# Kernel optimization log

Hardware: AMD Instinct MI355X
Metric: run time of the kernel (lower is better)

## Reference

```python
import jax, jax.numpy as jnp
import numpy as np

B, NQ, NKV, D, H, HD = 8, 1024, 2048, 1024, 16, 64  # inner_dim = H*HD = 1024


def setup_inputs() -> dict:
    key = jax.random.key(0)
    ks = jax.random.split(key, 10)
    s = 0.02
    return {
        "latent": jax.random.normal(ks[0], (B, NQ, D), jnp.float32),
        "data": jax.random.normal(ks[1], (B, NKV, D), jnp.float32),
        "wq": jax.random.normal(ks[2], (D, H * HD), jnp.float32) * s,
        "bq": jax.random.normal(ks[3], (H * HD,), jnp.float32) * s,
        "wk": jax.random.normal(ks[4], (D, H * HD), jnp.float32) * s,
        "bk": jax.random.normal(ks[5], (H * HD,), jnp.float32) * s,
        "wv": jax.random.normal(ks[6], (D, H * HD), jnp.float32) * s,
        "bv": jax.random.normal(ks[7], (H * HD,), jnp.float32) * s,
        "wo": jax.random.normal(ks[8], (H * HD, D), jnp.float32) * s,
        "bo": jax.random.normal(ks[9], (D,), jnp.float32) * s,
    }


def reference(latent, data, wq, bq, wk, bk, wv, bv, wo, bo):
    scale = HD ** -0.5
    # projections: [b, n, H*HD] -> [b, h, n, d]
    def split_heads(t):
        b, n, _ = t.shape
        return t.reshape(b, n, H, HD).transpose(0, 2, 1, 3)

    q = split_heads(latent @ wq + bq)   # [b, h, nq, d]
    k = split_heads(data @ wk + bk)     # [b, h, nkv, d]
    v = split_heads(data @ wv + bv)     # [b, h, nkv, d]

    scores = jnp.einsum("bhid,bhjd->bhij", q, k) * scale  # [b, h, nq, nkv]
    att = jax.nn.softmax(scores, axis=-1)                  # dropout p=0 (eval)
    out = jnp.einsum("bhij,bhjd->bhid", att, v)            # [b, h, nq, d]
    out = out.transpose(0, 2, 1, 3).reshape(B, NQ, H * HD)
    return out @ wo + bo
```

## Files before the change

### kernel.cpp

```cpp
#include <hip/hip_runtime.h>
#include <hip/hip_bf16.h>
#include <math.h>


using short8  = __attribute__((ext_vector_type(8))) short;
using f32x4   = __attribute__((ext_vector_type(4))) float;
using uint4v  = __attribute__((ext_vector_type(4))) unsigned int;

__device__ __forceinline__ ushort f2bf(float f) {
    unsigned u = __builtin_bit_cast(unsigned, f);
    u = (u + 0x7FFFu + ((u >> 16) & 1u)) >> 16;
    return (ushort)u;
}
__device__ __forceinline__ unsigned pack_bf2(float lo, float hi) {
    unsigned ulo = __builtin_bit_cast(unsigned, lo) + 0x8000u;
    unsigned uhi = __builtin_bit_cast(unsigned, hi) + 0x8000u;
    return __builtin_amdgcn_perm(uhi, ulo, 0x07060302);
}

__device__ __forceinline__ void gld_lds16(const ushort* g, ushort* l) {
    __builtin_amdgcn_global_load_lds(
        (const __attribute__((address_space(1))) unsigned int*)(const void*)g,
        (__attribute__((address_space(3))) unsigned int*)(void*)l,
        16, 0, 0);
}

__global__ void cvt_bf16(const float* __restrict__ in, ushort* __restrict__ out, int n) {
    int i = (blockIdx.x * blockDim.x + threadIdx.x) * 8;
    if (i >= n) return;
    float4 a = *(const float4*)(in + i);
    float4 b = *(const float4*)(in + i + 4);
    short8 o;
    o[0] = (short)f2bf(a.x); o[1] = (short)f2bf(a.y);
    o[2] = (short)f2bf(a.z); o[3] = (short)f2bf(a.w);
    o[4] = (short)f2bf(b.x); o[5] = (short)f2bf(b.y);
    o[6] = (short)f2bf(b.z); o[7] = (short)f2bf(b.w);
    *(short8*)(out + i) = o;
}

__global__ void transpose_w(const float* __restrict__ w0, const float* __restrict__ w1,
                            const float* __restrict__ w2, const float* __restrict__ w3,
                            ushort* __restrict__ o0, ushort* __restrict__ o1,
                            ushort* __restrict__ o2, ushort* __restrict__ o3) {
    __shared__ ushort tile[32][33];
    int z = blockIdx.z;
    const float* in = (z == 0) ? w0 : (z == 1) ? w1 : (z == 2) ? w2 : w3;
    ushort* out     = (z == 0) ? o0 : (z == 1) ? o1 : (z == 2) ? o2 : o3;
    int tx = threadIdx.x, ty = threadIdx.y;
    int x = blockIdx.x * 32 + tx;
    int y = blockIdx.y * 32;
#pragma unroll
    for (int i = 0; i < 32; i += 8)
        tile[ty + i][tx] = f2bf(in[(size_t)(y + ty + i) * 1024 + x]);
    __syncthreads();
    int x2 = blockIdx.y * 32 + tx;
    int y2 = blockIdx.x * 32;
#pragma unroll
    for (int i = 0; i < 32; i += 8)
        out[(size_t)(y2 + ty + i) * 1024 + x2] = tile[tx][ty + i];
}

template <int S>
__device__ __forceinline__ void stage_half(const ushort* __restrict__ G, int rbase,
                                           ushort* tile, int H, int kcol,
                                           int wave, int lane) {
#pragma unroll
    for (int c = 0; c < 2; ++c) {
        int rho = c * 64 + wave * 8;
        int gr0 = (rho / S) * (2 * S) + H * S + (rho % S);
        int rig = lane >> 3;
        int q   = (lane & 7) ^ rig;
        gld_lds16(G + (size_t)(rbase + gr0 + rig) * 1024 + kcol + q * 8,
                  tile + gr0 * 64);
    }
}

__device__ __forceinline__ void gemm256_body(
        const ushort* __restrict__ A, const ushort* __restrict__ Bt,
        const float* __restrict__ bias, void* __restrict__ Cv,
        float scale, int mode, int bm, int bn) {
    __shared__ __align__(16) ushort sm[65536];
    ushort* As0 = sm;
    ushort* Bs0 = sm + 16384;
    ushort* As1 = sm + 32768;
    ushort* Bs1 = sm + 49152;

    const int tid  = threadIdx.x;
    const int wave = tid >> 6, lane = tid & 63;
    const int l15 = lane & 15, quad = lane >> 4;
    const int wm = wave >> 2, wn = wave & 3;
    const int m0 = bm * 256, n0 = bn * 256;

    const int rA  = wm * 128 + l15;
    const int rB  = wn * 64 + l15;
    const int cq0 = quad ^ (l15 & 7);
    const int cq1 = (4 + quad) ^ (l15 & 7);

    stage_half<64>(A,  m0, As0, 0, 0,  wave, lane);
    stage_half<32>(Bt, n0, Bs0, 0, 0,  wave, lane);
    stage_half<32>(Bt, n0, Bs0, 1, 0,  wave, lane);
    stage_half<64>(A,  m0, As0, 1, 0,  wave, lane);
    stage_half<64>(A,  m0, As1, 0, 64, wave, lane);
    stage_half<32>(Bt, n0, Bs1, 1, 64, wave, lane);
    stage_half<64>(A,  m0, As1, 1, 64, wave, lane);
    asm volatile("s_waitcnt vmcnt(6)" ::: "memory");
    __builtin_amdgcn_s_barrier();

    f32x4 acc[8][4] = {};

#define LDA(MH)                                                                   \
    _Pragma("unroll")                                                             \
    for (int mi = 0; mi < 4; ++mi) {                                              \
        a[mi][0] = *(const short8*)(Ac + (rA + (MH) * 64 + mi * 16) * 64 + cq0 * 8); \
        a[mi][1] = *(const short8*)(Ac + (rA + (MH) * 64 + mi * 16) * 64 + cq1 * 8); \
    }
#define LDB(NH)                                                                   \
    _Pragma("unroll")                                                             \
    for (int ni = 0; ni < 2; ++ni) {                                              \
        b[ni][0] = *(const short8*)(Bc + (rB + (NH) * 32 + ni * 16) * 64 + cq0 * 8); \
        b[ni][1] = *(const short8*)(Bc + (rB + (NH) * 32 + ni * 16) * 64 + cq1 * 8); \
    }
#define MFMA_PHASE(MB, NB)                                                        \
    __builtin_amdgcn_s_barrier();                                                 \
    asm volatile("s_waitcnt lgkmcnt(0)" ::: "memory");                            \
    __builtin_amdgcn_sched_barrier(0);                                            \
    __builtin_amdgcn_s_setprio(1);                                                \
    _Pragma("unroll")                                                             \
    for (int mi = 0; mi < 4; ++mi)                                                \
        _Pragma("unroll")                                                         \
        for (int ni = 0; ni < 2; ++ni)                                            \
            _Pragma("unroll")                                                     \
            for (int kk = 0; kk < 2; ++kk)                                        \
                acc[(MB) * 4 + mi][(NB) * 2 + ni] =                               \
                    __builtin_amdgcn_mfma_f32_16x16x32_bf16(                      \
                        a[mi][kk], b[ni][kk], acc[(MB) * 4 + mi][(NB) * 2 + ni],  \
                        0, 0, 0);                                                 \
    __builtin_amdgcn_s_setprio(0);                                                \
    __builtin_amdgcn_s_barrier();

#pragma unroll 2
    for (int g = 0; g < 16; ++g) {
        ushort* Ac = (g & 1) ? As1 : As0;
        ushort* Bc = (g & 1) ? Bs1 : Bs0;
        ushort* Bn = (g & 1) ? Bs0 : Bs1;
        const int k1 = ((g + 1) & 15) * 64;
        const int k2 = ((g + 2) & 15) * 64;
        short8 a[4][2], b[2][2];

        LDA(0) LDB(0)
        stage_half<32>(Bt, n0, Bn, 0, k1, wave, lane);
        MFMA_PHASE(0, 0)

        LDB(1)
        stage_half<64>(A, m0, Ac, 0, k2, wave, lane);
        MFMA_PHASE(0, 1)

        LDA(1)
        stage_half<32>(Bt, n0, Bc, 1, k2, wave, lane);
        MFMA_PHASE(1, 1)

        LDB(0)
        stage_half<64>(A, m0, Ac, 1, k2, wave, lane);
        asm volatile("s_waitcnt vmcnt(6)" ::: "memory");
        MFMA_PHASE(1, 0)
    }
#undef LDA
#undef LDB
#undef MFMA_PHASE

    asm volatile("s_waitcnt vmcnt(0)" ::: "memory");

    float bvv[4];
    int   cols[4];
#pragma unroll
    for (int n4 = 0; n4 < 4; ++n4) {
        cols[n4] = n0 + wn * 64 + n4 * 16 + l15;
        bvv[n4]  = bias[cols[n4]];
    }
#pragma unroll
    for (int m8 = 0; m8 < 8; ++m8) {
        int rbase = m0 + wm * 128 + m8 * 16 + quad * 4;
#pragma unroll
        for (int n4 = 0; n4 < 4; ++n4) {
            float v[4];
#pragma unroll
            for (int rr = 0; rr < 4; ++rr)
                v[rr] = (acc[m8][n4][rr] + bvv[n4]) * scale;
            if (mode == 1) {
                int kvl = rbase & 2047;
                int pos = (kvl & ~31) + ((kvl >> 2) & 3) * 8 + ((kvl >> 4) & 1) * 4;
                size_t base = ((size_t)((rbase >> 11) * 1024 + cols[n4])) * 2048 + pos;
                uint2 o;
                o.x = pack_bf2(v[0], v[1]);
                o.y = pack_bf2(v[2], v[3]);
                *(uint2*)((ushort*)Cv + base) = o;
            } else if (mode == 0) {
#pragma unroll
                for (int rr = 0; rr < 4; ++rr)
                    ((ushort*)Cv)[(size_t)(rbase + rr) * 1024 + cols[n4]] = f2bf(v[rr]);
            } else {
#pragma unroll
                for (int rr = 0; rr < 4; ++rr)
                    ((float*)Cv)[(size_t)(rbase + rr) * 1024 + cols[n4]] = v[rr];
            }
        }
    }
}

__global__ __launch_bounds__(512, 2) void proj_qkv(
        const ushort* __restrict__ latB, const ushort* __restrict__ datB,
        const ushort* __restrict__ wqT, const ushort* __restrict__ wkT,
        const ushort* __restrict__ wvT,
        const float* __restrict__ bq, const float* __restrict__ bk,
        const float* __restrict__ bv,
        ushort* __restrict__ Qb, ushort* __restrict__ Kb, ushort* __restrict__ Vtb,
        float qscale) {
    int bid = ((int)blockIdx.x & 7) * 80 + ((int)blockIdx.x >> 3);
    const ushort* A;
    const ushort* W;
    const float*  bias;
    void*         C;
    float sc;
    int mode, idx;
    if (bid < 128)      { A = latB; W = wqT; bias = bq; C = Qb;  sc = qscale; mode = 0; idx = bid; }
    else if (bid < 384) { A = datB; W = wkT; bias = bk; C = Kb;  sc = 1.f;    mode = 0; idx = bid - 128; }
    else                { A = datB; W = wvT; bias = bv; C = Vtb; sc = 1.f;    mode = 1; idx = bid - 384; }
    gemm256_body(A, W, bias, C, sc, mode, idx >> 2, idx & 3);
}

template <int MODE>
__global__ void gemm_bt(const ushort* __restrict__ A, const ushort* __restrict__ Bt,
                        const float* __restrict__ bias, void* __restrict__ Cv,
                        int K, float scale) {
    __shared__ __align__(16) ushort As[128 * 32];
    __shared__ __align__(16) ushort Bs[128 * 32];
    const int tid  = threadIdx.x;
    const int wave = tid >> 6, lane = tid & 63;
    const int l15 = lane & 15, quad = lane >> 4;
    const int wm = wave & 1, wn = wave >> 1;
    const int m0 = blockIdx.x * 128;
    const int n0 = blockIdx.y * 128;

    f32x4 acc[4][4] = {};

    for (int k0 = 0; k0 < K; k0 += 32) {
        __syncthreads();
#pragma unroll
        for (int i = 0; i < 2; ++i) {
            int f   = (i * 256 + tid) * 8;
            int row = f >> 5, col = f & 31;
            gld_lds16(A  + (size_t)(m0 + row) * K + k0 + col, As + (i * 256 + wave * 64) * 8);
            gld_lds16(Bt + (size_t)(n0 + row) * K + k0 + col, Bs + (i * 256 + wave * 64) * 8);
        }
        __syncthreads();

        short8 a[4], b[4];
#pragma unroll
        for (int mi = 0; mi < 4; ++mi)
            a[mi] = *(const short8*)(As + (wm * 64 + mi * 16 + l15) * 32 + quad * 8);
#pragma unroll
        for (int ni = 0; ni < 4; ++ni)
            b[ni] = *(const short8*)(Bs + (wn * 64 + ni * 16 + l15) * 32 + quad * 8);
#pragma unroll
        for (int mi = 0; mi < 4; ++mi)
#pragma unroll
            for (int ni = 0; ni < 4; ++ni)
                acc[mi][ni] = __builtin_amdgcn_mfma_f32_16x16x32_bf16(a[mi], b[ni], acc[mi][ni], 0, 0, 0);
    }

    float bv[4];
    int   cols[4];
#pragma unroll
    for (int ni = 0; ni < 4; ++ni) {
        cols[ni] = n0 + wn * 64 + ni * 16 + l15;
        bv[ni]   = bias[cols[ni]];
    }
#pragma unroll
    for (int mi = 0; mi < 4; ++mi) {
        int rbase = m0 + wm * 64 + mi * 16 + quad * 4;
#pragma unroll
        for (int ni = 0; ni < 4; ++ni) {
            float v[4];
#pragma unroll
            for (int rr = 0; rr < 4; ++rr)
                v[rr] = (acc[mi][ni][rr] + bv[ni]) * scale;
            if (MODE == 1) {
                int kvl = rbase & 2047;
                int pos = (kvl & ~31) + ((kvl >> 2) & 3) * 8 + ((kvl >> 4) & 1) * 4;
                size_t base = ((size_t)((rbase >> 11) * 1024 + cols[ni])) * 2048 + pos;
                uint2 o;
                o.x = pack_bf2(v[0], v[1]);
                o.y = pack_bf2(v[2], v[3]);
                *(uint2*)((ushort*)Cv + base) = o;
            } else {
#pragma unroll
                for (int rr = 0; rr < 4; ++rr) {
                    int row = rbase + rr;
                    if (MODE == 0)
                        ((ushort*)Cv)[(size_t)row * 1024 + cols[ni]] = f2bf(v[rr]);
                    else
                        ((float*)Cv)[(size_t)row * 1024 + cols[ni]] = v[rr];
                }
            }
        }
    }
}

__global__ __launch_bounds__(256, 4) void attn_fused(const ushort* __restrict__ Q,
                                                     const ushort* __restrict__ K,
                                                     const ushort* __restrict__ Vt,
                                                     ushort* __restrict__ O) {
    __shared__ __align__(16) ushort smem[2 * 8192];
    ushort* Ks  = smem;
    ushort* Vts = smem + 8192;

    const int tid  = threadIdx.x;
    const int wave = tid >> 6, lane = tid & 63;
    const int l15 = lane & 15, quad = lane >> 4;
    const int bx = blockIdx.x;
    const int bh = bx & 127, h = bh & 15, b = bh >> 4;
    const int q0 = (bx >> 7) * 128;

    const ushort* Qg = Q + ((size_t)(b * 1024 + q0)) * 1024 + h * 64;
    const ushort* Kg = K + ((size_t)(b * 2048)) * 1024 + h * 64;
    const ushort* Vg = Vt + ((size_t)(b * 1024 + h * 64)) * 2048;

    short8 bq[2][2];
#pragma unroll
    for (int qt = 0; qt < 2; ++qt) {
        int row = wave * 32 + qt * 16 + l15;
#pragma unroll
        for (int ks = 0; ks < 2; ++ks)
            bq[ks][qt] = *(const short8*)(Qg + (size_t)row * 1024 + ks * 32 + quad * 8);
    }

    f32x4 Oacc[4][2] = {};
    float l_run[2] = {0.f, 0.f};

    const int rig = lane >> 3;
    const int scb8 = (lane & 7) ^ rig;
    const int riv = lane >> 4;
    const int cb16 = lane & 15;

    for (int kv0 = 0; kv0 < 2048; kv0 += 128) {
        __syncthreads();
#pragma unroll
        for (int g = 0; g < 4; ++g) {
            int G = wave * 4 + g;
            gld_lds16(Kg + (size_t)(kv0 + G * 8 + rig) * 1024 + scb8 * 8, Ks + G * 512);
            int vrow = G * 4 + riv;
            int scv = cb16 ^ (vrow & 15);
            gld_lds16(Vg + (size_t)vrow * 2048 + kv0 + scv * 8, Vts + G * 512);
        }
        __syncthreads();

        unsigned pk[8][2][2];
#pragma unroll
        for (int kvt = 0; kvt < 8; ++kvt) {
            f32x4 s0 = {}, s1 = {};
#pragma unroll
            for (int ks = 0; ks < 2; ++ks) {
                int ck = ((ks * 4 + quad) ^ (l15 & 7)) * 8;
                short8 ak = *(const short8*)(Ks + (kvt * 16 + l15) * 64 + ck);
                s0 = __builtin_amdgcn_mfma_f32_16x16x32_bf16(ak, bq[ks][0], s0, 0, 0, 0);
                s1 = __builtin_amdgcn_mfma_f32_16x16x32_bf16(ak, bq[ks][1], s1, 0, 0, 0);
            }
            float p0[4], p1[4];
#pragma unroll
            for (int rr = 0; rr < 4; ++rr) {
                p0[rr] = __builtin_amdgcn_exp2f(s0[rr]);
                p1[rr] = __builtin_amdgcn_exp2f(s1[rr]);
                l_run[0] += p0[rr];
                l_run[1] += p1[rr];
            }
            pk[kvt][0][0] = pack_bf2(p0[0], p0[1]);
            pk[kvt][0][1] = pack_bf2(p0[2], p0[3]);
            pk[kvt][1][0] = pack_bf2(p1[0], p1[1]);
            pk[kvt][1][1] = pack_bf2(p1[2], p1[3]);
        }

#pragma unroll
        for (int sp = 0; sp < 4; ++sp) {
#pragma unroll
            for (int dt = 0; dt < 4; ++dt) {
                int cv = ((sp * 4 + quad) ^ l15) * 8;
                short8 av = *(const short8*)(Vts + (dt * 16 + l15) * 128 + cv);
#pragma unroll
                for (int qt = 0; qt < 2; ++qt) {
                    uint4v u = {pk[2 * sp][qt][0], pk[2 * sp][qt][1],
                                pk[2 * sp + 1][qt][0], pk[2 * sp + 1][qt][1]};
                    short8 bp = __builtin_bit_cast(short8, u);
                    Oacc[dt][qt] = __builtin_amdgcn_mfma_f32_16x16x32_bf16(av, bp, Oacc[dt][qt], 0, 0, 0);
                }
            }
        }
    }

#pragma unroll
    for (int qt = 0; qt < 2; ++qt) {
        float l = l_run[qt];
        l += __shfl_xor(l, 16);
        l += __shfl_xor(l, 32);
        float inv = 1.f / l;
        int qg = q0 + wave * 32 + qt * 16 + l15;
#pragma unroll
        for (int dt = 0; dt < 4; ++dt) {
            uint2 o;
            o.x = pack_bf2(Oacc[dt][qt][0] * inv, Oacc[dt][qt][1] * inv);
            o.y = pack_bf2(Oacc[dt][qt][2] * inv, Oacc[dt][qt][3] * inv);
            *(uint2*)(O + ((size_t)(b * 1024 + qg)) * 1024 + h * 64 + dt * 16 + quad * 4) = o;
        }
    }
}

extern "C" void kernel_launch(void* const* d_in, const int* in_sizes, int n_in,
                              void* d_out, int out_size, void* d_ws, size_t ws_size,
                              hipStream_t stream) {
    const float* latent = (const float*)d_in[0];
    const float* data   = (const float*)d_in[1];
    const float* wq     = (const float*)d_in[2];
    const float* bq     = (const float*)d_in[3];
    const float* wk     = (const float*)d_in[4];
    const float* bk     = (const float*)d_in[5];
    const float* wv     = (const float*)d_in[6];
    const float* bv     = (const float*)d_in[7];
    const float* wo     = (const float*)d_in[8];
    const float* bo     = (const float*)d_in[9];
    float* out = (float*)d_out;

    ushort* ws   = (ushort*)d_ws;
    ushort* wqT  = ws;
    ushort* wkT  = wqT + (1u << 20);
    ushort* wvT  = wkT + (1u << 20);
    ushort* woT  = wvT + (1u << 20);
    ushort* latB = woT + (1u << 20);
    ushort* datB = latB + (8u << 20);
    ushort* Qb   = datB + (16u << 20);
    ushort* Kb   = Qb + (8u << 20);
    ushort* Vtb  = Kb + (16u << 20);
    ushort* AO   = Vtb + (16u << 20);

    cvt_bf16<<<(8u << 20) / (256 * 8), 256, 0, stream>>>(latent, latB, 8u << 20);
    cvt_bf16<<<(16u << 20) / (256 * 8), 256, 0, stream>>>(data, datB, 16u << 20);
    transpose_w<<<dim3(32, 32, 4), dim3(32, 8), 0, stream>>>(wq, wk, wv, wo, wqT, wkT, wvT, woT);

    const float qscale = 0.125f * 1.44269504088896340736f;
    proj_qkv<<<dim3(640), 512, 0, stream>>>(latB, datB, wqT, wkT, wvT,
                                            bq, bk, bv, Qb, Kb, Vtb, qscale);
    attn_fused<<<dim3(1024), 256, 0, stream>>>(Qb, Kb, Vtb, AO);
    gemm_bt<2><<<dim3(64, 8), 256, 0, stream>>>(AO, woT, bo, out, 1024, 1.0f);
}
```

Before: 364.1 us.

## Register-prefetch K/V tiles in attention and fuse prep kernels into one launch

The attention kernel stops using direct global-to-LDS loads. It now loads the next K/V tile into registers during compute and writes them to LDS at the top of the next iteration, so global latency overlaps the MFMA work. Launch bounds drop from 4 to 3 blocks per SM to make room for the extra registers. The three preprocessing kernels (two bf16 conversions and the weight transposes) are merged into one launch, and the attention output buffer reuses the latent bf16 buffer to shrink the workspace. The costs are lower occupancy and an extra register round trip per tile.

```diff
diff --git a/kernel.cpp b/kernel.cpp
--- a/kernel.cpp
+++ b/kernel.cpp
@@ -25,36 +25,45 @@
         16, 0, 0);
 }
 
-__global__ void cvt_bf16(const float* __restrict__ in, ushort* __restrict__ out, int n) {
-    int i = (blockIdx.x * blockDim.x + threadIdx.x) * 8;
-    if (i >= n) return;
-    float4 a = *(const float4*)(in + i);
-    float4 b = *(const float4*)(in + i + 4);
-    short8 o;
-    o[0] = (short)f2bf(a.x); o[1] = (short)f2bf(a.y);
-    o[2] = (short)f2bf(a.z); o[3] = (short)f2bf(a.w);
-    o[4] = (short)f2bf(b.x); o[5] = (short)f2bf(b.y);
-    o[6] = (short)f2bf(b.z); o[7] = (short)f2bf(b.w);
-    *(short8*)(out + i) = o;
-}
-
-__global__ void transpose_w(const float* __restrict__ w0, const float* __restrict__ w1,
-                            const float* __restrict__ w2, const float* __restrict__ w3,
-                            ushort* __restrict__ o0, ushort* __restrict__ o1,
-                            ushort* __restrict__ o2, ushort* __restrict__ o3) {
+__global__ void prep_fused(const float* __restrict__ latent, const float* __restrict__ data,
+                           const float* __restrict__ wq, const float* __restrict__ wk,
+                           const float* __restrict__ wv, const float* __restrict__ wo,
+                           ushort* __restrict__ latB, ushort* __restrict__ datB,
+                           ushort* __restrict__ wqT, ushort* __restrict__ wkT,
+                           ushort* __restrict__ wvT, ushort* __restrict__ woT) {
     __shared__ ushort tile[32][33];
-    int z = blockIdx.z;
-    const float* in = (z == 0) ? w0 : (z == 1) ? w1 : (z == 2) ? w2 : w3;
-    ushort* out     = (z == 0) ? o0 : (z == 1) ? o1 : (z == 2) ? o2 : o3;
-    int tx = threadIdx.x, ty = threadIdx.y;
-    int x = blockIdx.x * 32 + tx;
-    int y = blockIdx.y * 32;
+    const int bx  = blockIdx.x;
+    const int tid = threadIdx.x;
+    if (bx < 12288) {
+        const float* in = (bx < 4096) ? latent : data;
+        ushort* out     = (bx < 4096) ? latB : datB;
+        int idx = (bx < 4096) ? bx : bx - 4096;
+        int i = (idx * 256 + tid) * 8;
+        float4 a = *(const float4*)(in + i);
+        float4 b = *(const float4*)(in + i + 4);
+        short8 o;
+        o[0] = (short)f2bf(a.x); o[1] = (short)f2bf(a.y);
+        o[2] = (short)f2bf(a.z); o[3] = (short)f2bf(a.w);
+        o[4] = (short)f2bf(b.x); o[5] = (short)f2bf(b.y);
+        o[6] = (short)f2bf(b.z); o[7] = (short)f2bf(b.w);
+        *(short8*)(out + i) = o;
+        return;
+    }
+    int rem = bx - 12288;
+    int z   = rem >> 10;
+    int bxx = rem & 31;
+    int byy = (rem >> 5) & 31;
+    const float* in = (z == 0) ? wq : (z == 1) ? wk : (z == 2) ? wv : wo;
+    ushort* out     = (z == 0) ? wqT : (z == 1) ? wkT : (z == 2) ? wvT : woT;
+    int tx = tid & 31, ty = tid >> 5;
+    int x = bxx * 32 + tx;
+    int y = byy * 32;
 #pragma unroll
     for (int i = 0; i < 32; i += 8)
         tile[ty + i][tx] = f2bf(in[(size_t)(y + ty + i) * 1024 + x]);
     __syncthreads();
-    int x2 = blockIdx.y * 32 + tx;
-    int y2 = blockIdx.x * 32;
+    int x2 = byy * 32 + tx;
+    int y2 = bxx * 32;
 #pragma unroll
     for (int i = 0; i < 32; i += 8)
         out[(size_t)(y2 + ty + i) * 1024 + x2] = tile[tx][ty + i];
@@ -306,7 +315,7 @@
     }
 }
 
-__global__ __launch_bounds__(256, 4) void attn_fused(const ushort* __restrict__ Q,
+__global__ __launch_bounds__(256, 3) void attn_fused(const ushort* __restrict__ Q,
                                                      const ushort* __restrict__ K,
                                                      const ushort* __restrict__ Vt,
                                                      ushort* __restrict__ O) {
@@ -342,17 +351,37 @@
     const int riv = lane >> 4;
     const int cb16 = lane & 15;
 
+    short8 kreg[4], vreg[4];
+#pragma unroll
+    for (int g = 0; g < 4; ++g) {
+        int G = wave * 4 + g;
+        kreg[g] = *(const short8*)(Kg + (size_t)(G * 8 + rig) * 1024 + scb8 * 8);
+        int vrow = G * 4 + riv;
+        int scv = cb16 ^ (vrow & 15);
+        vreg[g] = *(const short8*)(Vg + (size_t)vrow * 2048 + scv * 8);
+    }
+
     for (int kv0 = 0; kv0 < 2048; kv0 += 128) {
         __syncthreads();
 #pragma unroll
         for (int g = 0; g < 4; ++g) {
             int G = wave * 4 + g;
-            gld_lds16(Kg + (size_t)(kv0 + G * 8 + rig) * 1024 + scb8 * 8, Ks + G * 512);
-            int vrow = G * 4 + riv;
-            int scv = cb16 ^ (vrow & 15);
-            gld_lds16(Vg + (size_t)vrow * 2048 + kv0 + scv * 8, Vts + G * 512);
+            *(short8*)(Ks  + G * 512 + lane * 8) = kreg[g];
+            *(short8*)(Vts + G * 512 + lane * 8) = vreg[g];
         }
         __syncthreads();
+
+        if (kv0 + 128 < 2048) {
+            int kvn = kv0 + 128;
+#pragma unroll
+            for (int g = 0; g < 4; ++g) {
+                int G = wave * 4 + g;
+                kreg[g] = *(const short8*)(Kg + (size_t)(kvn + G * 8 + rig) * 1024 + scb8 * 8);
+                int vrow = G * 4 + riv;
+                int scv = cb16 ^ (vrow & 15);
+                vreg[g] = *(const short8*)(Vg + (size_t)vrow * 2048 + kvn + scv * 8);
+            }
+        }
 
         unsigned pk[8][2][2];
 #pragma unroll
@@ -438,11 +467,10 @@
     ushort* Qb   = datB + (16u << 20);
     ushort* Kb   = Qb + (8u << 20);
     ushort* Vtb  = Kb + (16u << 20);
-    ushort* AO   = Vtb + (16u << 20);
-
-    cvt_bf16<<<(8u << 20) / (256 * 8), 256, 0, stream>>>(latent, latB, 8u << 20);
-    cvt_bf16<<<(16u << 20) / (256 * 8), 256, 0, stream>>>(data, datB, 16u << 20);
-    transpose_w<<<dim3(32, 32, 4), dim3(32, 8), 0, stream>>>(wq, wk, wv, wo, wqT, wkT, wvT, woT);
+    ushort* AO   = latB;
+
+    prep_fused<<<dim3(16384), 256, 0, stream>>>(latent, data, wq, wk, wv, wo,
+                                                latB, datB, wqT, wkT, wvT, woT);
 
     const float qscale = 0.125f * 1.44269504088896340736f;
     proj_qkv<<<dim3(640), 512, 0, stream>>>(latB, datB, wqT, wkT, wvT,
```

Result: slower. 371.6 us (+2.1%).
